# Kernel optimization log

Measured on AMD Instinct MI355X. Metric: run time of the kernel, lower is better.

The kernel has to match this reference:

```python
import jax, jax.numpy as jnp
import numpy as np

P = 16          # patch size
IMG = 384       # image size
D = 768         # model dim
DM = 3072       # mlp hidden
L = 12          # n blocks
H = 12          # n heads
DH = D // H     # head dim
NC = 1000       # n classes
B = 64          # batch
N = (IMG // P) ** 2  # 576 patches


def layernorm(x, w, b, eps=1e-5):
    m = jnp.mean(x, axis=-1, keepdims=True)
    v = jnp.mean((x - m) ** 2, axis=-1, keepdims=True)
    return (x - m) / jnp.sqrt(v + eps) * w + b


def gelu(x):
    return jax.nn.gelu(x, approximate=False)  # torch nn.GELU default (erf)


def setup_inputs() -> dict:
    key = jax.random.key(0)
    ks = iter(jax.random.split(key, 40))
    nrm = lambda shape, s=0.02: jax.random.normal(next(ks), shape, jnp.float32) * s
    return {
        "x": jax.random.normal(next(ks), (B, 3, IMG, IMG), jnp.float32),
        "class_embed": nrm((D,)),
        "pose_embed": nrm((N + 1, D)),
        "proj_w": nrm((3 * P * P, D)), "proj_b": jnp.zeros((D,), jnp.float32),
        "qkv_w": nrm((L, D, 3 * D)), "qkv_b": jnp.zeros((L, 3 * D), jnp.float32),
        "top_w": nrm((L, D, D)), "top_b": jnp.zeros((L, D), jnp.float32),
        "ln1_w": jnp.ones((L, D), jnp.float32), "ln1_b": jnp.zeros((L, D), jnp.float32),
        "ln2_w": jnp.ones((L, D), jnp.float32), "ln2_b": jnp.zeros((L, D), jnp.float32),
        "mlp_w1": nrm((L, D, DM)), "mlp_b1": jnp.zeros((L, DM), jnp.float32),
        "mlp_w2": nrm((L, DM, D)), "mlp_b2": jnp.zeros((L, D), jnp.float32),
        "ln3_w": jnp.ones((D,), jnp.float32), "ln3_b": jnp.zeros((D,), jnp.float32),
        "head_w1": nrm((D, DM)), "head_b1": jnp.zeros((DM,), jnp.float32),
        "head_w2": nrm((DM, NC)), "head_b2": jnp.zeros((NC,), jnp.float32),
    }


def reference(x, class_embed, pose_embed, proj_w, proj_b, qkv_w, qkv_b,
              top_w, top_b, ln1_w, ln1_b, ln2_w, ln2_b,
              mlp_w1, mlp_b1, mlp_w2, mlp_b2, ln3_w, ln3_b,
              head_w1, head_b1, head_w2, head_b2):
    Bx = x.shape[0]
    # _slice_patch: torch unfold(dim2).unfold(dim3) -> (B,C,N,P,P) -> permute -> flatten (C,Ph,Pw order)
    patches = x.reshape(Bx, 3, IMG // P, P, IMG // P, P)
    patches = patches.transpose(0, 2, 4, 1, 3, 5).reshape(Bx, N, 3 * P * P)
    patch_embed = patches @ proj_w + proj_b  # (B, N, D)
    cls = jnp.broadcast_to(class_embed, (Bx, 1, D))
    z = jnp.concatenate([cls, patch_embed], axis=1) + pose_embed  # (B, N+1, D)

    scale = DH ** 0.5
    for i in range(L):
        # MSA branch (note: source computes attention over the HEAD axis per token, HxH)
        h = layernorm(z, ln1_w[i], ln1_b[i])
        qkv = h @ qkv_w[i] + qkv_b[i]
        q, k, v = jnp.split(qkv, 3, axis=-1)
        q = q.reshape(Bx, N + 1, H, DH)
        k = k.reshape(Bx, N + 1, H, DH)
        v = v.reshape(Bx, N + 1, H, DH)
        A = jax.nn.softmax(jnp.einsum('bnhd,bngd->bnhg', q, k) / scale, axis=-1)
        o = jnp.einsum('bnhg,bngd->bnhd', A, v).reshape(Bx, N + 1, D)
        z = o @ top_w[i] + top_b[i] + z
        # MLP branch (GELU after both linears, per source MLP)
        h2 = layernorm(z, ln2_w[i], ln2_b[i])
        m = gelu(gelu(h2 @ mlp_w1[i] + mlp_b1[i]) @ mlp_w2[i] + mlp_b2[i])
        z = m + z

    y = layernorm(z[:, 0], ln3_w, ln3_b)  # (B, D)
    logit = gelu(gelu(y @ head_w1 + head_b1) @ head_w2 + head_b2)  # pretraining cls_head = MLP
    return logit
```

## Files before the change

### kernel.cpp

```cpp
#include <hip/hip_runtime.h>

typedef unsigned short u16;
typedef unsigned int u32;
typedef __bf16 bf16x8 __attribute__((ext_vector_type(8)));
typedef float f32x4 __attribute__((ext_vector_type(4)));

#define D_    768
#define DM_   3072
#define NL_   12
#define NT_   577
#define NP_   576
#define B_    64
#define MREAL (B_*NT_)
#define MPAD2 37120
#define NC_   1000
#define IMG_  384

__device__ __forceinline__ float bf2f(u16 v){
  union { unsigned u; float f; } c; c.u = ((unsigned)v) << 16; return c.f;
}
__device__ __forceinline__ u16 f2bf(float f){
  union { float f; unsigned u; } c; c.f = f;
  unsigned r = c.u + 0x7FFFu + ((c.u >> 16) & 1u);
  return (u16)(r >> 16);
}
__device__ __forceinline__ float gelu_f(float x){
  return 0.5f * x * (1.0f + erff(x * 0.70710678118654752f));
}
__device__ __forceinline__ void gload16(const void* g, void* l){
  __builtin_amdgcn_global_load_lds((const __attribute__((address_space(1))) void*)g,
                                   (__attribute__((address_space(3))) void*)l, 16, 0, 0);
}

#define SB_ __builtin_amdgcn_sched_barrier(0)

template<int EPI>
__global__ __launch_bounds__(512, 1) void gemm256_k(
    const u16* __restrict__ A, const u16* __restrict__ Bt,
    const float* __restrict__ bias, const float* __restrict__ res,
    void* __restrict__ outv, int K, int ldo, int nbn)
{
  __shared__ u16 lds[2][2][256*64];
  const int tid = threadIdx.x;
  const int l   = tid & 63;
  const int wid = tid >> 6;
  const int wm  = wid >> 2, wn = wid & 3;
  const int lrow = l & 15;

  const int nwg = gridDim.x;
  const int q = nwg >> 3, r = nwg & 7;
  const int xcd = blockIdx.x & 7, o = blockIdx.x >> 3;
  const int wg = (xcd < r ? xcd * (q + 1) : r * (q + 1) + (xcd - r) * q) + o;
  const int bm = wg / nbn, bn = wg % nbn;

  const int cs8 = ((tid & 7) ^ ((tid >> 3) & 7)) * 8;
  const int rb  = tid >> 3;
  const u16* aP[4]; const u16* bP[4];
  #pragma unroll
  for (int i = 0; i < 4; i++) {
    aP[i] = A  + (size_t)(bm*256 + rb + 64*i) * K + cs8;
    bP[i] = Bt + (size_t)(bn*256 + rb + 64*i) * K + cs8;
  }
  const int ldst = tid * 8;

  f32x4 acc[8][4];
  #pragma unroll
  for (int i = 0; i < 8; i++)
    #pragma unroll
    for (int j = 0; j < 4; j++) acc[i][j] = {0.f, 0.f, 0.f, 0.f};

  const int nk = K >> 6;
  #pragma unroll
  for (int i = 0; i < 4; i++) {
    gload16(aP[i], &lds[0][0][ldst + i*4096]);
    gload16(bP[i], &lds[0][1][ldst + i*4096]);
    aP[i] += 64; bP[i] += 64;
  }

  const int sw  = (lrow & 7) << 4;
  const int g16 = (l >> 4) << 4;

  for (int t = 0; t < nk; ++t) {
    const int cur = t & 1;
    const bool pre = (t + 1 < nk);
    u16* dA = &lds[cur^1][0][0];
    u16* dB = &lds[cur^1][1][0];

    if (pre) {
      gload16(aP[0], dA + ldst);
      gload16(aP[1], dA + ldst + 4096);
    }
    SB_;
    if (pre) asm volatile("s_waitcnt vmcnt(2)" ::: "memory");
    else     asm volatile("s_waitcnt vmcnt(0)" ::: "memory");
    SB_;
    __builtin_amdgcn_s_barrier();
    SB_;

    const char* As_ = (const char*)&lds[cur][0][0];
    const char* Bs_ = (const char*)&lds[cur][1][0];
    bf16x8 af[4], bfr[4];

    {
      const int kb = g16;
      #pragma unroll
      for (int ni = 0; ni < 4; ni++)
        bfr[ni] = *(const bf16x8*)(Bs_ + ((wn*64 + ni*16 + lrow) << 7) + (kb ^ sw));
      #pragma unroll
      for (int mi = 0; mi < 4; mi++)
        af[mi] = *(const bf16x8*)(As_ + ((wm*128 + mi*16 + lrow) << 7) + (kb ^ sw));
      if (pre) {
        gload16(aP[2], dA + ldst + 8192);
        gload16(aP[3], dA + ldst + 12288);
      }
      asm volatile("s_waitcnt lgkmcnt(0)" ::: "memory");
      SB_;
      __builtin_amdgcn_s_setprio(1);
      #pragma unroll
      for (int mi = 0; mi < 4; mi++)
        #pragma unroll
        for (int ni = 0; ni < 4; ni++)
          acc[mi][ni] = __builtin_amdgcn_mfma_f32_16x16x32_bf16(af[mi], bfr[ni], acc[mi][ni], 0, 0, 0);
      __builtin_amdgcn_s_setprio(0);
      SB_;
      __builtin_amdgcn_s_barrier();
      SB_;
    }
    {
      const int kb = g16;
      #pragma unroll
      for (int mi = 0; mi < 4; mi++)
        af[mi] = *(const bf16x8*)(As_ + ((wm*128 + (mi+4)*16 + lrow) << 7) + (kb ^ sw));
      if (pre) {
        gload16(bP[0], dB + ldst);
        gload16(bP[1], dB + ldst + 4096);
      }
      asm volatile("s_waitcnt lgkmcnt(0)" ::: "memory");
      SB_;
      __builtin_amdgcn_s_setprio(1);
      #pragma unroll
      for (int mi = 0; mi < 4; mi++)
        #pragma unroll
        for (int ni = 0; ni < 4; ni++)
          acc[mi+4][ni] = __builtin_amdgcn_mfma_f32_16x16x32_bf16(af[mi], bfr[ni], acc[mi+4][ni], 0, 0, 0);
      __builtin_amdgcn_s_setprio(0);
      SB_;
      __builtin_amdgcn_s_barrier();
      SB_;
    }
    {
      const int kb = 64 | g16;
      #pragma unroll
      for (int ni = 0; ni < 4; ni++)
        bfr[ni] = *(const bf16x8*)(Bs_ + ((wn*64 + ni*16 + lrow) << 7) + (kb ^ sw));
      #pragma unroll
      for (int mi = 0; mi < 4; mi++)
        af[mi] = *(const bf16x8*)(As_ + ((wm*128 + mi*16 + lrow) << 7) + (kb ^ sw));
      if (pre) {
        gload16(bP[2], dB + ldst + 8192);
        gload16(bP[3], dB + ldst + 12288);
      }
      asm volatile("s_waitcnt lgkmcnt(0)" ::: "memory");
      SB_;
      __builtin_amdgcn_s_setprio(1);
      #pragma unroll
      for (int mi = 0; mi < 4; mi++)
        #pragma unroll
        for (int ni = 0; ni < 4; ni++)
          acc[mi][ni] = __builtin_amdgcn_mfma_f32_16x16x32_bf16(af[mi], bfr[ni], acc[mi][ni], 0, 0, 0);
      __builtin_amdgcn_s_setprio(0);
      SB_;
      __builtin_amdgcn_s_barrier();
      SB_;
    }
    {
      const int kb = 64 | g16;
      #pragma unroll
      for (int mi = 0; mi < 4; mi++)
        af[mi] = *(const bf16x8*)(As_ + ((wm*128 + (mi+4)*16 + lrow) << 7) + (kb ^ sw));
      asm volatile("s_waitcnt lgkmcnt(0)" ::: "memory");
      SB_;
      __builtin_amdgcn_s_setprio(1);
      #pragma unroll
      for (int mi = 0; mi < 4; mi++)
        #pragma unroll
        for (int ni = 0; ni < 4; ni++)
          acc[mi+4][ni] = __builtin_amdgcn_mfma_f32_16x16x32_bf16(af[mi], bfr[ni], acc[mi+4][ni], 0, 0, 0);
      __builtin_amdgcn_s_setprio(0);
      SB_;
      __builtin_amdgcn_s_barrier();
      SB_;
    }
    if (pre) {
      #pragma unroll
      for (int i = 0; i < 4; i++) { aP[i] += 64; bP[i] += 64; }
    }
  }

  const int orow0 = bm*256 + wm*128;
  const int ocol0 = bn*256 + wn*64;
  #pragma unroll
  for (int mi = 0; mi < 8; mi++) {
    #pragma unroll
    for (int ni = 0; ni < 4; ni++) {
      const int col = ocol0 + ni*16 + (l & 15);
      const float bv = bias[col];
      #pragma unroll
      for (int r2 = 0; r2 < 4; r2++) {
        const int row = orow0 + mi*16 + (l >> 4)*4 + r2;
        const float v = acc[mi][ni][r2] + bv;
        const size_t idx = (size_t)row * ldo + col;
        if constexpr (EPI == 0) ((u16*)outv)[idx] = f2bf(v);
        else if constexpr (EPI == 1) ((float*)outv)[idx] = v + res[idx];
        else if constexpr (EPI == 2) ((u16*)outv)[idx] = f2bf(gelu_f(v));
        else if constexpr (EPI == 3) ((float*)outv)[idx] = gelu_f(v) + res[idx];
        else if constexpr (EPI == 4) ((float*)outv)[idx] = v;
      }
    }
  }
}

template<int EPI>
__global__ __launch_bounds__(256) void gemm_k(
    const u16* __restrict__ A, const u16* __restrict__ Bt,
    const float* __restrict__ bias, const float* __restrict__ res,
    void* __restrict__ outv, int K, int ldo, int nbn, int Ms, int Ns)
{
  __shared__ u16 As[128*64];
  __shared__ u16 Bs[128*64];
  const int tid = threadIdx.x;
  const int l   = tid & 63;
  const int w   = tid >> 6;
  const int wm  = w >> 1, wn = w & 1;
  const int lrow = l & 15;

  const int nwg = gridDim.x;
  const int q = nwg >> 3, r = nwg & 7;
  const int xcd = blockIdx.x & 7, o = blockIdx.x >> 3;
  const int wg = (xcd < r ? xcd * (q + 1) : r * (q + 1) + (xcd - r) * q) + o;
  const int bm = wg / nbn, bn = wg % nbn;

  const int cs8 = ((tid & 7) ^ ((tid >> 3) & 7)) * 8;
  const int rb  = tid >> 3;
  const size_t abase = (size_t)bm * 128 * K;
  const size_t bbase = (size_t)bn * 128 * K;
  size_t aoff[4], boff[4];
  #pragma unroll
  for (int i = 0; i < 4; i++) {
    aoff[i] = abase + (size_t)(rb + 32 * i) * K + cs8;
    boff[i] = bbase + (size_t)(rb + 32 * i) * K + cs8;
  }

  const int colA = (l >> 4) << 4;
  const int sw   = (lrow & 7) << 4;

  f32x4 acc[4][4];
  #pragma unroll
  for (int i = 0; i < 4; i++)
    #pragma unroll
    for (int j = 0; j < 4; j++) acc[i][j] = {0.f, 0.f, 0.f, 0.f};

  const int nk = K >> 6;
  for (int kt = 0; kt < nk; ++kt) {
    const int koff = kt * 64;
    #pragma unroll
    for (int i = 0; i < 4; i++) {
      gload16(A  + aoff[i] + koff, As + tid * 8 + i * 2048);
      gload16(Bt + boff[i] + koff, Bs + tid * 8 + i * 2048);
    }
    __syncthreads();
    #pragma unroll
    for (int kk = 0; kk < 2; kk++) {
      bf16x8 af[4], bfr[4];
      #pragma unroll
      for (int mi = 0; mi < 4; mi++)
        af[mi] = *(const bf16x8*)((const char*)As +
                  ((wm*64 + mi*16 + lrow) << 7) + (((kk << 6) | colA) ^ sw));
      #pragma unroll
      for (int ni = 0; ni < 4; ni++)
        bfr[ni] = *(const bf16x8*)((const char*)Bs +
                  ((wn*64 + ni*16 + lrow) << 7) + (((kk << 6) | colA) ^ sw));
      #pragma unroll
      for (int mi = 0; mi < 4; mi++)
        #pragma unroll
        for (int ni = 0; ni < 4; ni++)
          acc[mi][ni] = __builtin_amdgcn_mfma_f32_16x16x32_bf16(af[mi], bfr[ni], acc[mi][ni], 0, 0, 0);
    }
    __syncthreads();
  }

  const int orow0 = bm*128 + wm*64;
  const int ocol0 = bn*128 + wn*64;
  #pragma unroll
  for (int mi = 0; mi < 4; mi++) {
    #pragma unroll
    for (int ni = 0; ni < 4; ni++) {
      #pragma unroll
      for (int r2 = 0; r2 < 4; r2++) {
        const int row = orow0 + mi*16 + (l >> 4)*4 + r2;
        const int col = ocol0 + ni*16 + (l & 15);
        float bv;
        if constexpr (EPI == 5) bv = (col < Ns) ? bias[col] : 0.f;
        else bv = bias[col];
        const float v = acc[mi][ni][r2] + bv;
        const size_t idx = (size_t)row * ldo + col;
        if constexpr (EPI == 2) ((u16*)outv)[idx] = f2bf(gelu_f(v));
        else if constexpr (EPI == 5) {
          if (row < Ms && col < Ns) ((float*)outv)[(size_t)row * Ns + col] = gelu_f(v);
        }
      }
    }
  }
}

__global__ void wconv_k(const float* __restrict__ W, u16* __restrict__ Wt,
                        int K, int N)
{
  __shared__ float tile[32][33];
  const int n0 = blockIdx.x * 32, k0 = blockIdx.y * 32;
  const int tx = threadIdx.x, ty = threadIdx.y;
  #pragma unroll
  for (int r = 0; r < 4; r++) {
    const int kk = k0 + ty + r*8;
    const int nn = n0 + tx;
    tile[ty + r*8][tx] = (nn < N) ? W[(size_t)kk * N + nn] : 0.f;
  }
  __syncthreads();
  #pragma unroll
  for (int r = 0; r < 4; r++) {
    const int nn = n0 + ty + r*8;
    Wt[(size_t)nn * K + k0 + tx] = f2bf(tile[tx][ty + r*8]);
  }
}

__global__ void patchify_k(const float* __restrict__ x, u16* __restrict__ hb)
{
  const int blk = blockIdx.x;
  const int b = blk / NP_, p = blk % NP_;
  const int pr = p / 24, pc = p % 24;
  const size_t row = (size_t)b * NT_ + 1 + p;
  #pragma unroll
  for (int u = 0; u < 3; u++) {
    const int j  = threadIdx.x + u * 256;
    const int c  = j >> 8, ph = (j >> 4) & 15, pw = j & 15;
    const float v = x[((size_t)(b*3 + c) * IMG_ + pr*16 + ph) * IMG_ + pc*16 + pw];
    hb[row * D_ + j] = f2bf(v);
  }
}

__global__ void posecls_k(float* __restrict__ z, const float* __restrict__ ce,
                          const float* __restrict__ pe)
{
  const int row = blockIdx.x;
  const int t = row % NT_;
  const size_t base = (size_t)row * D_;
  #pragma unroll
  for (int u = 0; u < 3; u++) {
    const int j = threadIdx.x + u * 256;
    if (t == 0) z[base + j] = ce[j] + pe[j];
    else        z[base + j] += pe[(size_t)t * D_ + j];
  }
}

__global__ void ln_k(const float* __restrict__ z, const float* __restrict__ w,
                     const float* __restrict__ b, u16* __restrict__ out)
{
  const int row = blockIdx.x * 4 + (threadIdx.x >> 6);
  const int l = threadIdx.x & 63;
  const float4* zr = (const float4*)(z + (size_t)row * D_);
  float4 xq[3];
  float s = 0.f;
  #pragma unroll
  for (int j = 0; j < 3; j++) {
    xq[j] = zr[j*64 + l];
    s += xq[j].x + xq[j].y + xq[j].z + xq[j].w;
  }
  #pragma unroll
  for (int m = 1; m < 64; m <<= 1) s += __shfl_xor(s, m, 64);
  const float mean = s * (1.0f / 768.0f);
  float ss = 0.f;
  #pragma unroll
  for (int j = 0; j < 3; j++) {
    const float dx = xq[j].x-mean, dy = xq[j].y-mean, dz = xq[j].z-mean, dw = xq[j].w-mean;
    ss += dx*dx + dy*dy + dz*dz + dw*dw;
  }
  #pragma unroll
  for (int m = 1; m < 64; m <<= 1) ss += __shfl_xor(ss, m, 64);
  const float rinv = rsqrtf(ss * (1.0f / 768.0f) + 1e-5f);
  const size_t ob = (size_t)row * D_;
  #pragma unroll
  for (int j = 0; j < 3; j++) {
    const int c = (j*64 + l) * 4;
    const float4 wv = *(const float4*)(w + c);
    const float4 bv = *(const float4*)(b + c);
    ushort4 ov;
    ov.x = f2bf((xq[j].x - mean) * rinv * wv.x + bv.x);
    ov.y = f2bf((xq[j].y - mean) * rinv * wv.y + bv.y);
    ov.z = f2bf((xq[j].z - mean) * rinv * wv.z + bv.z);
    ov.w = f2bf((xq[j].w - mean) * rinv * wv.w + bv.w);
    *(ushort4*)(out + ob + c) = ov;
  }
}

__global__ void lncls_k(const float* __restrict__ z, const float* __restrict__ w,
                        const float* __restrict__ b, u16* __restrict__ out)
{
  const int row = blockIdx.x * 4 + (threadIdx.x >> 6);
  const int l = threadIdx.x & 63;
  const size_t ob = (size_t)row * D_;
  if (row >= B_) {
    #pragma unroll
    for (int j = 0; j < 12; j++) out[ob + j*64 + l] = 0;
    return;
  }
  const float* zr = z + (size_t)row * NT_ * D_;
  float xv[12];
  float s = 0.f;
  #pragma unroll
  for (int j = 0; j < 12; j++) { xv[j] = zr[j*64 + l]; s += xv[j]; }
  #pragma unroll
  for (int m = 1; m < 64; m <<= 1) s += __shfl_xor(s, m, 64);
  const float mean = s * (1.0f / 768.0f);
  float ss = 0.f;
  #pragma unroll
  for (int j = 0; j < 12; j++) { const float d = xv[j] - mean; ss += d * d; }
  #pragma unroll
  for (int m = 1; m < 64; m <<= 1) ss += __shfl_xor(ss, m, 64);
  const float rinv = rsqrtf(ss * (1.0f / 768.0f) + 1e-5f);
  #pragma unroll
  for (int j = 0; j < 12; j++) {
    const int cidx = j*64 + l;
    out[ob + cidx] = f2bf((xv[j] - mean) * rinv * w[cidx] + b[cidx]);
  }
}

__global__ __launch_bounds__(256) void attn_k(const u16* __restrict__ qkv,
                                              u16* __restrict__ o)
{
  const int tok = (blockIdx.x * 256 + threadIdx.x) >> 6;
  const int l  = threadIdx.x & 63;
  const int g  = l >> 4, li = l & 15;
  const size_t rb = (size_t)tok * (3 * D_);

  f32x4 s = {0.f, 0.f, 0.f, 0.f};
  #pragma unroll
  for (int kt = 0; kt < 2; kt++) {
    const bf16x8 ka = *(const bf16x8*)(qkv + rb + D_ + li*64 + g*8 + kt*32);
    const bf16x8 qb = *(const bf16x8*)(qkv + rb +      li*64 + g*8 + kt*32);
    s = __builtin_amdgcn_mfma_f32_16x16x32_bf16(ka, qb, s, 0, 0, 0);
  }

  float sv[4];
  #pragma unroll
  for (int r2 = 0; r2 < 4; r2++) sv[r2] = s[r2] * 0.125f;
  float mx = (g < 3) ? fmaxf(fmaxf(sv[0], sv[1]), fmaxf(sv[2], sv[3])) : -1e30f;
  mx = fmaxf(mx, __shfl_xor(mx, 16, 64));
  mx = fmaxf(mx, __shfl_xor(mx, 32, 64));
  float p[4], den = 0.f;
  #pragma unroll
  for (int r2 = 0; r2 < 4; r2++) {
    p[r2] = (g < 3) ? __expf(sv[r2] - mx) : 0.f;
    den += p[r2];
  }
  den += __shfl_xor(den, 16, 64);
  den += __shfl_xor(den, 32, 64);
  const float rden = 1.0f / den;
  #pragma unroll
  for (int r2 = 0; r2 < 4; r2++) p[r2] *= rden;

  const u32 pk01 = ((u32)f2bf(p[1]) << 16) | f2bf(p[0]);
  const u32 pk23 = ((u32)f2bf(p[3]) << 16) | f2bf(p[2]);

  const int srcA = (li + (g << 5)) & 63;
  const int srcB = (srcA + 16) & 63;
  u32 b0 = (u32)__shfl((int)pk01, srcA, 64);
  u32 b1 = (u32)__shfl((int)pk23, srcA, 64);
  u32 b2 = (u32)__shfl((int)pk01, srcB, 64);
  u32 b3 = (u32)__shfl((int)pk23, srcB, 64);
  if (g >= 2) { b0 = 0; b1 = 0; b2 = 0; b3 = 0; }
  union { u32 u[4]; bf16x8 v; } pb;
  pb.u[0] = b0; pb.u[1] = b1; pb.u[2] = b2; pb.u[3] = b3;

  const size_t ob = (size_t)tok * D_;
  #pragma unroll
  for (int t = 0; t < 4; t++) {
    union { u16 a[8]; bf16x8 v; } va;
    #pragma unroll
    for (int jp = 0; jp < 8; jp++) {
      const int j = g * 8 + jp;
      va.a[jp] = (j < 12) ? qkv[rb + 2*D_ + j*64 + t*16 + li] : (u16)0;
    }
    f32x4 oac = {0.f, 0.f, 0.f, 0.f};
    oac = __builtin_amdgcn_mfma_f32_16x16x32_bf16(va.v, pb.v, oac, 0, 0, 0);
    if (li < 12) {
      ushort4 ov;
      ov.x = f2bf(oac[0]); ov.y = f2bf(oac[1]);
      ov.z = f2bf(oac[2]); ov.w = f2bf(oac[3]);
      *(ushort4*)(o + ob + li*64 + t*16 + g*4) = ov;
    }
  }
}

extern "C" void kernel_launch(void* const* d_in, const int* in_sizes, int n_in,
                              void* d_out, int out_size, void* d_ws, size_t ws_size,
                              hipStream_t stream)
{
  const float* x    = (const float*)d_in[0];
  const float* ce   = (const float*)d_in[1];
  const float* pe   = (const float*)d_in[2];
  const float* pw   = (const float*)d_in[3];
  const float* pb   = (const float*)d_in[4];
  const float* qkvw = (const float*)d_in[5];
  const float* qkvb = (const float*)d_in[6];
  const float* topw = (const float*)d_in[7];
  const float* topb = (const float*)d_in[8];
  const float* l1w  = (const float*)d_in[9];
  const float* l1b  = (const float*)d_in[10];
  const float* l2w  = (const float*)d_in[11];
  const float* l2b  = (const float*)d_in[12];
  const float* w1   = (const float*)d_in[13];
  const float* b1   = (const float*)d_in[14];
  const float* w2   = (const float*)d_in[15];
  const float* b2   = (const float*)d_in[16];
  const float* l3w  = (const float*)d_in[17];
  const float* l3b  = (const float*)d_in[18];
  const float* hw1  = (const float*)d_in[19];
  const float* hb1  = (const float*)d_in[20];
  const float* hw2  = (const float*)d_in[21];
  const float* hb2  = (const float*)d_in[22];

  char* ws = (char*)d_ws;
  constexpr size_t SZ_Z  = (size_t)MPAD2 * D_ * 4;
  constexpr size_t SZ_HB = (size_t)MPAD2 * D_ * 2;
  constexpr size_t SZ_QM = (size_t)MPAD2 * DM_ * 2;
  constexpr size_t SZ_WB = (size_t)DM_ * 1024 * 2;
  constexpr size_t SZ_YB = (size_t)128 * D_ * 2;
  float* z  = (float*)ws;
  u16*   hb = (u16*)(ws + SZ_Z);
  u16*   qm = (u16*)(ws + SZ_Z + SZ_HB);
  u16*   wb = (u16*)(ws + SZ_Z + SZ_HB + SZ_QM);
  u16*   yb = (u16*)(ws + SZ_Z + SZ_HB + SZ_QM + SZ_WB);
  u16*   t1 = (u16*)(ws + SZ_Z + SZ_HB + SZ_QM + SZ_WB + SZ_YB);

  const dim3 blk(256);
  const dim3 blk5(512);
  const dim3 wblk(32, 8);
  const int MT2 = MPAD2 / 256;

  patchify_k<<<B_ * NP_, blk, 0, stream>>>(x, hb);
  wconv_k<<<dim3(D_/32, D_/32), wblk, 0, stream>>>(pw, wb, D_, D_);
  gemm256_k<4><<<3*MT2, blk5, 0, stream>>>(hb, wb, pb, nullptr, z, D_, D_, 3);
  posecls_k<<<MREAL, blk, 0, stream>>>(z, ce, pe);

  for (int i = 0; i < NL_; i++) {
    ln_k<<<MPAD2/4, blk, 0, stream>>>(z, l1w + i*D_, l1b + i*D_, hb);
    wconv_k<<<dim3(3*D_/32, D_/32), wblk, 0, stream>>>(qkvw + (size_t)i*D_*3*D_, wb, D_, 3*D_);
    gemm256_k<0><<<9*MT2, blk5, 0, stream>>>(hb, wb, qkvb + i*3*D_, nullptr, qm, D_, 3*D_, 9);
    attn_k<<<MREAL/4, blk, 0, stream>>>(qm, hb);
    wconv_k<<<dim3(D_/32, D_/32), wblk, 0, stream>>>(topw + (size_t)i*D_*D_, wb, D_, D_);
    gemm256_k<1><<<3*MT2, blk5, 0, stream>>>(hb, wb, topb + i*D_, z, z, D_, D_, 3);
    ln_k<<<MPAD2/4, blk, 0, stream>>>(z, l2w + i*D_, l2b + i*D_, hb);
    wconv_k<<<dim3(DM_/32, D_/32), wblk, 0, stream>>>(w1 + (size_t)i*D_*DM_, wb, D_, DM_);
    gemm256_k<2><<<12*MT2, blk5, 0, stream>>>(hb, wb, b1 + i*DM_, nullptr, qm, D_, DM_, 12);
    wconv_k<<<dim3(D_/32, DM_/32), wblk, 0, stream>>>(w2 + (size_t)i*DM_*D_, wb, DM_, D_);
    gemm256_k<3><<<3*MT2, blk5, 0, stream>>>(qm, wb, b2 + i*D_, z, z, DM_, D_, 3);
  }

  lncls_k<<<32, blk, 0, stream>>>(z, l3w, l3b, yb);
  wconv_k<<<dim3(DM_/32, D_/32), wblk, 0, stream>>>(hw1, wb, D_, DM_);
  gemm_k<2><<<24, blk, 0, stream>>>(yb, wb, hb1, nullptr, t1, D_, DM_, 24, 0, 0);
  wconv_k<<<dim3(1024/32, DM_/32), wblk, 0, stream>>>(hw2, wb, DM_, NC_);
  gemm_k<5><<<8, blk, 0, stream>>>(t1, wb, hb2, nullptr, (float*)d_out, DM_, 1024, 8, B_, NC_);
}
```

Before: 11.24 ms.

## Emit LayerNorm output in MFMA-fragment packed layout and load A directly to registers

LayerNorm now writes its bf16 output in a pre-packed layout matching the MFMA 16x32 A-fragment order, so the QKV and MLP-up GEMMs can load A straight from global memory into registers. This removes the A tile from LDS and halves LDS use and LDS traffic in those GEMMs. A fragments are double-buffered in registers across the k loop. The cost is more register pressure and uncoalesced-per-wave global loads for A with no LDS reuse across waves, and LayerNorm rereads z a second time.

Result: slower. 12.02 ms (+7.0%).

```diff
diff --git a/kernel.cpp b/kernel.cpp
--- a/kernel.cpp
+++ b/kernel.cpp
@@ -31,8 +31,132 @@
   __builtin_amdgcn_global_load_lds((const __attribute__((address_space(1))) void*)g,
                                    (__attribute__((address_space(3))) void*)l, 16, 0, 0);
 }
-
 #define SB_ __builtin_amdgcn_sched_barrier(0)
+
+template<int EPI>
+__global__ __launch_bounds__(512, 1) void gemmPA_k(
+    const u16* __restrict__ Apk, const u16* __restrict__ Bt,
+    const float* __restrict__ bias,
+    void* __restrict__ outv, int K, int ldo, int nbn)
+{
+  __shared__ u16 Bs[2][16384];
+  const int tid = threadIdx.x;
+  const int l   = tid & 63;
+  const int wid = tid >> 6;
+  const int wm  = wid >> 2, wn = wid & 3;
+  const int lrow = l & 15;
+
+  const int nwg = gridDim.x;
+  const int q = nwg >> 3, r = nwg & 7;
+  const int xcd = blockIdx.x & 7, o = blockIdx.x >> 3;
+  const int wg = (xcd < r ? xcd * (q + 1) : r * (q + 1) + (xcd - r) * q) + o;
+  const int bm = wg / nbn, bn = wg % nbn;
+
+  const int cs8 = ((tid & 7) ^ ((tid >> 3) & 7)) * 8;
+  const int rb  = tid >> 3;
+  const u16* bP[4];
+  #pragma unroll
+  for (int i = 0; i < 4; i++)
+    bP[i] = Bt + (size_t)(bn*256 + rb + 64*i) * K + cs8;
+  const int ldst = tid * 8;
+
+  const int KT = K >> 5;
+  const u16* aBase = Apk + (size_t)(bm*16 + wm*8) * KT * 512 + (size_t)l * 8;
+
+  const int sw  = (lrow & 7) << 4;
+  const int g16 = (l >> 4) << 4;
+
+  f32x4 acc[8][4];
+  #pragma unroll
+  for (int i = 0; i < 8; i++)
+    #pragma unroll
+    for (int j = 0; j < 4; j++) acc[i][j] = {0.f, 0.f, 0.f, 0.f};
+
+  const int nk = K >> 6;
+
+  #pragma unroll
+  for (int i = 0; i < 4; i++) { gload16(bP[i], &Bs[0][ldst + i*4096]); bP[i] += 64; }
+  bf16x8 Ae[8], Ao[8];
+  #pragma unroll
+  for (int mi = 0; mi < 8; mi++) Ae[mi] = *(const bf16x8*)(aBase + ((size_t)mi*KT + 0)*512);
+  #pragma unroll
+  for (int mi = 0; mi < 8; mi++) Ao[mi] = *(const bf16x8*)(aBase + ((size_t)mi*KT + 1)*512);
+
+  for (int t = 0; t < nk; ++t) {
+    const int cur = t & 1;
+    const bool pre = (t + 1 < nk);
+    if (pre) {
+      #pragma unroll
+      for (int i = 0; i < 4; i++) { gload16(bP[i], &Bs[cur^1][ldst + i*4096]); bP[i] += 64; }
+    }
+    SB_;
+    if (pre) asm volatile("s_waitcnt vmcnt(20)" ::: "memory");
+    else     asm volatile("s_waitcnt vmcnt(16)" ::: "memory");
+    SB_;
+    __builtin_amdgcn_s_barrier();
+    SB_;
+    const char* Bb = (const char*)&Bs[cur][0];
+    bf16x8 bfr[4];
+    #pragma unroll
+    for (int ni = 0; ni < 4; ni++)
+      bfr[ni] = *(const bf16x8*)(Bb + ((wn*64 + ni*16 + lrow) << 7) + (g16 ^ sw));
+    asm volatile("s_waitcnt lgkmcnt(0)" ::: "memory");
+    SB_;
+    __builtin_amdgcn_s_setprio(1);
+    #pragma unroll
+    for (int mi = 0; mi < 8; mi++)
+      #pragma unroll
+      for (int ni = 0; ni < 4; ni++)
+        acc[mi][ni] = __builtin_amdgcn_mfma_f32_16x16x32_bf16(Ae[mi], bfr[ni], acc[mi][ni], 0, 0, 0);
+    __builtin_amdgcn_s_setprio(0);
+    SB_;
+    if (pre) {
+      #pragma unroll
+      for (int mi = 0; mi < 8; mi++)
+        Ae[mi] = *(const bf16x8*)(aBase + ((size_t)mi*KT + 2*(t+1))*512);
+    }
+    #pragma unroll
+    for (int ni = 0; ni < 4; ni++)
+      bfr[ni] = *(const bf16x8*)(Bb + ((wn*64 + ni*16 + lrow) << 7) + ((64 | g16) ^ sw));
+    asm volatile("s_waitcnt lgkmcnt(0)" ::: "memory");
+    SB_;
+    __builtin_amdgcn_s_setprio(1);
+    #pragma unroll
+    for (int mi = 0; mi < 8; mi++)
+      #pragma unroll
+      for (int ni = 0; ni < 4; ni++)
+        acc[mi][ni] = __builtin_amdgcn_mfma_f32_16x16x32_bf16(Ao[mi], bfr[ni], acc[mi][ni], 0, 0, 0);
+    __builtin_amdgcn_s_setprio(0);
+    SB_;
+    if (pre) {
+      #pragma unroll
+      for (int mi = 0; mi < 8; mi++)
+        Ao[mi] = *(const bf16x8*)(aBase + ((size_t)mi*KT + 2*(t+1) + 1)*512);
+    }
+    SB_;
+    __builtin_amdgcn_s_barrier();
+    SB_;
+  }
+
+  const int orow0 = bm*256 + wm*128;
+  const int ocol0 = bn*256 + wn*64;
+  #pragma unroll
+  for (int mi = 0; mi < 8; mi++) {
+    #pragma unroll
+    for (int ni = 0; ni < 4; ni++) {
+      const int col = ocol0 + ni*16 + (l & 15);
+      const float bv = bias[col];
+      #pragma unroll
+      for (int r2 = 0; r2 < 4; r2++) {
+        const int row = orow0 + mi*16 + (l >> 4)*4 + r2;
+        const float v = acc[mi][ni][r2] + bv;
+        const size_t idx = (size_t)row * ldo + col;
+        if constexpr (EPI == 0) ((u16*)outv)[idx] = f2bf(v);
+        else if constexpr (EPI == 2) ((u16*)outv)[idx] = f2bf(gelu_f(v));
+      }
+    }
+  }
+}
 
 template<int EPI>
 __global__ __launch_bounds__(512, 1) void gemm256_k(
@@ -210,9 +334,7 @@
         const int row = orow0 + mi*16 + (l >> 4)*4 + r2;
         const float v = acc[mi][ni][r2] + bv;
         const size_t idx = (size_t)row * ldo + col;
-        if constexpr (EPI == 0) ((u16*)outv)[idx] = f2bf(v);
-        else if constexpr (EPI == 1) ((float*)outv)[idx] = v + res[idx];
-        else if constexpr (EPI == 2) ((u16*)outv)[idx] = f2bf(gelu_f(v));
+        if constexpr (EPI == 1) ((float*)outv)[idx] = v + res[idx];
         else if constexpr (EPI == 3) ((float*)outv)[idx] = gelu_f(v) + res[idx];
         else if constexpr (EPI == 4) ((float*)outv)[idx] = v;
       }
@@ -362,43 +484,66 @@
   }
 }
 
-__global__ void ln_k(const float* __restrict__ z, const float* __restrict__ w,
-                     const float* __restrict__ b, u16* __restrict__ out)
-{
-  const int row = blockIdx.x * 4 + (threadIdx.x >> 6);
-  const int l = threadIdx.x & 63;
-  const float4* zr = (const float4*)(z + (size_t)row * D_);
-  float4 xq[3];
-  float s = 0.f;
-  #pragma unroll
-  for (int j = 0; j < 3; j++) {
-    xq[j] = zr[j*64 + l];
-    s += xq[j].x + xq[j].y + xq[j].z + xq[j].w;
-  }
-  #pragma unroll
-  for (int m = 1; m < 64; m <<= 1) s += __shfl_xor(s, m, 64);
-  const float mean = s * (1.0f / 768.0f);
-  float ss = 0.f;
-  #pragma unroll
-  for (int j = 0; j < 3; j++) {
-    const float dx = xq[j].x-mean, dy = xq[j].y-mean, dz = xq[j].z-mean, dw = xq[j].w-mean;
-    ss += dx*dx + dy*dy + dz*dz + dw*dw;
-  }
-  #pragma unroll
-  for (int m = 1; m < 64; m <<= 1) ss += __shfl_xor(ss, m, 64);
-  const float rinv = rsqrtf(ss * (1.0f / 768.0f) + 1e-5f);
-  const size_t ob = (size_t)row * D_;
-  #pragma unroll
-  for (int j = 0; j < 3; j++) {
-    const int c = (j*64 + l) * 4;
-    const float4 wv = *(const float4*)(w + c);
-    const float4 bv = *(const float4*)(b + c);
-    ushort4 ov;
-    ov.x = f2bf((xq[j].x - mean) * rinv * wv.x + bv.x);
-    ov.y = f2bf((xq[j].y - mean) * rinv * wv.y + bv.y);
-    ov.z = f2bf((xq[j].z - mean) * rinv * wv.z + bv.z);
-    ov.w = f2bf((xq[j].w - mean) * rinv * wv.w + bv.w);
-    *(ushort4*)(out + ob + c) = ov;
+__global__ void ln_pk(const float* __restrict__ z, const float* __restrict__ w,
+                      const float* __restrict__ b, u16* __restrict__ out)
+{
+  __shared__ float st[16][2];
+  const int blk = blockIdx.x;
+  const int tid = threadIdx.x;
+  const int l = tid & 63, w4 = tid >> 6;
+
+  for (int rr = 0; rr < 4; rr++) {
+    const int lr = w4*4 + rr;
+    const float4* zr = (const float4*)(z + ((size_t)blk*16 + lr) * D_);
+    float4 xq[3];
+    float s = 0.f;
+    #pragma unroll
+    for (int j = 0; j < 3; j++) {
+      xq[j] = zr[j*64 + l];
+      s += xq[j].x + xq[j].y + xq[j].z + xq[j].w;
+    }
+    #pragma unroll
+    for (int m = 1; m < 64; m <<= 1) s += __shfl_xor(s, m, 64);
+    const float mean = s * (1.0f / 768.0f);
+    float ss = 0.f;
+    #pragma unroll
+    for (int j = 0; j < 3; j++) {
+      const float dx = xq[j].x-mean, dy = xq[j].y-mean, dz = xq[j].z-mean, dw = xq[j].w-mean;
+      ss += dx*dx + dy*dy + dz*dz + dw*dw;
+    }
+    #pragma unroll
+    for (int m = 1; m < 64; m <<= 1) ss += __shfl_xor(ss, m, 64);
+    if (l == 0) {
+      st[lr][0] = mean;
+      st[lr][1] = rsqrtf(ss * (1.0f / 768.0f) + 1e-5f);
+    }
+  }
+  __syncthreads();
+
+  #pragma unroll
+  for (int i = 0; i < 6; i++) {
+    const int c = tid + i*256;
+    const int kt = c >> 6, lane = c & 63;
+    const int lr = lane & 15, g = (lane >> 4);
+    const int k0 = kt*32 + g*8;
+    const float* zp = z + ((size_t)blk*16 + lr) * D_ + k0;
+    const float4 a0 = *(const float4*)zp;
+    const float4 a1 = *(const float4*)(zp + 4);
+    const float4 w0 = *(const float4*)(w + k0);
+    const float4 w1 = *(const float4*)(w + k0 + 4);
+    const float4 b0 = *(const float4*)(b + k0);
+    const float4 b1 = *(const float4*)(b + k0 + 4);
+    const float mean = st[lr][0], rinv = st[lr][1];
+    u16 ov[8];
+    ov[0] = f2bf((a0.x - mean) * rinv * w0.x + b0.x);
+    ov[1] = f2bf((a0.y - mean) * rinv * w0.y + b0.y);
+    ov[2] = f2bf((a0.z - mean) * rinv * w0.z + b0.z);
+    ov[3] = f2bf((a0.w - mean) * rinv * w0.w + b0.w);
+    ov[4] = f2bf((a1.x - mean) * rinv * w1.x + b1.x);
+    ov[5] = f2bf((a1.y - mean) * rinv * w1.y + b1.y);
+    ov[6] = f2bf((a1.z - mean) * rinv * w1.z + b1.z);
+    ov[7] = f2bf((a1.w - mean) * rinv * w1.w + b1.w);
+    *(uint4*)(out + ((size_t)(blk*24 + kt)*64 + lane)*8) = *(const uint4*)ov;
   }
 }
 
@@ -553,15 +698,15 @@
   posecls_k<<<MREAL, blk, 0, stream>>>(z, ce, pe);
 
   for (int i = 0; i < NL_; i++) {
-    ln_k<<<MPAD2/4, blk, 0, stream>>>(z, l1w + i*D_, l1b + i*D_, hb);
+    ln_pk<<<MPAD2/16, blk, 0, stream>>>(z, l1w + i*D_, l1b + i*D_, hb);
     wconv_k<<<dim3(3*D_/32, D_/32), wblk, 0, stream>>>(qkvw + (size_t)i*D_*3*D_, wb, D_, 3*D_);
-    gemm256_k<0><<<9*MT2, blk5, 0, stream>>>(hb, wb, qkvb + i*3*D_, nullptr, qm, D_, 3*D_, 9);
+    gemmPA_k<0><<<9*MT2, blk5, 0, stream>>>(hb, wb, qkvb + i*3*D_, qm, D_, 3*D_, 9);
     attn_k<<<MREAL/4, blk, 0, stream>>>(qm, hb);
     wconv_k<<<dim3(D_/32, D_/32), wblk, 0, stream>>>(topw + (size_t)i*D_*D_, wb, D_, D_);
     gemm256_k<1><<<3*MT2, blk5, 0, stream>>>(hb, wb, topb + i*D_, z, z, D_, D_, 3);
-    ln_k<<<MPAD2/4, blk, 0, stream>>>(z, l2w + i*D_, l2b + i*D_, hb);
+    ln_pk<<<MPAD2/16, blk, 0, stream>>>(z, l2w + i*D_, l2b + i*D_, hb);
     wconv_k<<<dim3(DM_/32, D_/32), wblk, 0, stream>>>(w1 + (size_t)i*D_*DM_, wb, D_, DM_);
-    gemm256_k<2><<<12*MT2, blk5, 0, stream>>>(hb, wb, b1 + i*DM_, nullptr, qm, D_, DM_, 12);
+    gemmPA_k<2><<<12*MT2, blk5, 0, stream>>>(hb, wb, b1 + i*DM_, qm, D_, DM_, 12);
     wconv_k<<<dim3(D_/32, DM_/32), wblk, 0, stream>>>(w2 + (size_t)i*DM_*D_, wb, DM_, D_);
     gemm256_k<3><<<3*MT2, blk5, 0, stream>>>(qm, wb, b2 + i*D_, z, z, DM_, D_, 3);
   }
```

## Add 128x128 triple-buffered GEMM for QKV and MLP-up projections

Applied to the files above, without the earlier changes.

Adds a new 256-thread GEMM kernel with 128x128 tiles, a 3-slot LDS ring fed by direct global-to-LDS loads, swizzled LDS layout, and multiple workgroups per CU. QKV and first MLP GEMMs (bf16 output epilogues) switch from the 256x256 single-occupancy kernel to this one. The intent is to hide memory latency through deeper prefetch and higher occupancy. The trade-off is less operand reuse per tile, so more global and LDS traffic.

Result: no change. 11.33 ms (+0.8%).

```diff
diff --git a/kernel.cpp b/kernel.cpp
--- a/kernel.cpp
+++ b/kernel.cpp
@@ -31,8 +31,126 @@
   __builtin_amdgcn_global_load_lds((const __attribute__((address_space(1))) void*)g,
                                    (__attribute__((address_space(3))) void*)l, 16, 0, 0);
 }
-
 #define SB_ __builtin_amdgcn_sched_barrier(0)
+
+template<int EPI>
+__global__ __launch_bounds__(256, 3) void gemmR_k(
+    const u16* __restrict__ A, const u16* __restrict__ Bt,
+    const float* __restrict__ bias,
+    void* __restrict__ outv, int K, int ldo, int nbn)
+{
+  __shared__ u16 ring[3][2][4096];
+  const int tid = threadIdx.x;
+  const int l   = tid & 63;
+  const int w   = tid >> 6;
+  const int wm  = w >> 1, wn = w & 1;
+  const int lrow = l & 15;
+  const int g2   = l >> 4;
+
+  const int nwg = gridDim.x;
+  const int q = nwg >> 3, r = nwg & 7;
+  const int xcd = blockIdx.x & 7, o = blockIdx.x >> 3;
+  const int wg = (xcd < r ? xcd * (q + 1) : r * (q + 1) + (xcd - r) * q) + o;
+  const int bm = wg / nbn, bn = wg % nbn;
+
+  const int rp0  = tid >> 3;
+  const int rodd = (tid >> 2) & 1;
+  const int scol = ((tid & 3) ^ (rp0 & 3)) * 8;
+  const u16* aS[2]; const u16* bS[2];
+  #pragma unroll
+  for (int i = 0; i < 2; i++) {
+    const int row = (rp0 + 32*i) * 2 + rodd;
+    aS[i] = A  + (size_t)(bm*128 + row) * K + scol;
+    bS[i] = Bt + (size_t)(bn*128 + row) * K + scol;
+  }
+  const int dst = tid * 8;
+
+  int afo[4], bfo[4];
+  #pragma unroll
+  for (int mi = 0; mi < 4; mi++) {
+    const int ar = wm*64 + mi*16 + lrow;
+    afo[mi] = (ar >> 1)*128 + (ar & 1)*64 + ((g2 ^ ((ar >> 1) & 3)) << 4);
+    const int br = wn*64 + mi*16 + lrow;
+    bfo[mi] = (br >> 1)*128 + (br & 1)*64 + ((g2 ^ ((br >> 1) & 3)) << 4);
+  }
+
+  f32x4 acc[4][4];
+  #pragma unroll
+  for (int i = 0; i < 4; i++)
+    #pragma unroll
+    for (int j = 0; j < 4; j++) acc[i][j] = {0.f, 0.f, 0.f, 0.f};
+
+  const int nt = K >> 5;
+
+#define STG_R(t_) { \
+    const int sl_ = (t_) % 3; const int ko_ = (t_) * 32; \
+    gload16(aS[0] + ko_, &ring[sl_][0][dst]); \
+    gload16(aS[1] + ko_, &ring[sl_][0][dst + 2048]); \
+    gload16(bS[0] + ko_, &ring[sl_][1][dst]); \
+    gload16(bS[1] + ko_, &ring[sl_][1][dst + 2048]); }
+
+#define CMP_R(t_) { \
+    const int sl_ = (t_) % 3; \
+    const char* As_ = (const char*)&ring[sl_][0][0]; \
+    const char* Bs_ = (const char*)&ring[sl_][1][0]; \
+    bf16x8 af[4], bfr[4]; \
+    _Pragma("unroll") \
+    for (int mi = 0; mi < 4; mi++) af[mi]  = *(const bf16x8*)(As_ + afo[mi]); \
+    _Pragma("unroll") \
+    for (int ni = 0; ni < 4; ni++) bfr[ni] = *(const bf16x8*)(Bs_ + bfo[ni]); \
+    asm volatile("s_waitcnt lgkmcnt(0)" ::: "memory"); \
+    SB_; \
+    __builtin_amdgcn_s_setprio(1); \
+    _Pragma("unroll") \
+    for (int mi = 0; mi < 4; mi++) \
+      _Pragma("unroll") \
+      for (int ni = 0; ni < 4; ni++) \
+        acc[mi][ni] = __builtin_amdgcn_mfma_f32_16x16x32_bf16(af[mi], bfr[ni], acc[mi][ni], 0, 0, 0); \
+    __builtin_amdgcn_s_setprio(0); \
+    SB_; \
+    __builtin_amdgcn_s_barrier(); \
+    SB_; }
+
+  STG_R(0); STG_R(1);
+
+  for (int t = 0; t < nt - 2; ++t) {
+    STG_R(t + 2);
+    SB_;
+    asm volatile("s_waitcnt vmcnt(8)" ::: "memory");
+    SB_;
+    __builtin_amdgcn_s_barrier();
+    SB_;
+    CMP_R(t);
+  }
+  SB_; asm volatile("s_waitcnt vmcnt(4)" ::: "memory"); SB_;
+  __builtin_amdgcn_s_barrier(); SB_;
+  CMP_R(nt - 2);
+  SB_; asm volatile("s_waitcnt vmcnt(0)" ::: "memory"); SB_;
+  __builtin_amdgcn_s_barrier(); SB_;
+  CMP_R(nt - 1);
+
+#undef STG_R
+#undef CMP_R
+
+  const int orow0 = bm*128 + wm*64;
+  const int ocol0 = bn*128 + wn*64;
+  #pragma unroll
+  for (int mi = 0; mi < 4; mi++) {
+    #pragma unroll
+    for (int ni = 0; ni < 4; ni++) {
+      const int col = ocol0 + ni*16 + lrow;
+      const float bv = bias[col];
+      #pragma unroll
+      for (int r2 = 0; r2 < 4; r2++) {
+        const int row = orow0 + mi*16 + g2*4 + r2;
+        const float v = acc[mi][ni][r2] + bv;
+        const size_t idx = (size_t)row * ldo + col;
+        if constexpr (EPI == 0) ((u16*)outv)[idx] = f2bf(v);
+        else if constexpr (EPI == 2) ((u16*)outv)[idx] = f2bf(gelu_f(v));
+      }
+    }
+  }
+}
 
 template<int EPI>
 __global__ __launch_bounds__(512, 1) void gemm256_k(
@@ -210,9 +328,7 @@
         const int row = orow0 + mi*16 + (l >> 4)*4 + r2;
         const float v = acc[mi][ni][r2] + bv;
         const size_t idx = (size_t)row * ldo + col;
-        if constexpr (EPI == 0) ((u16*)outv)[idx] = f2bf(v);
-        else if constexpr (EPI == 1) ((float*)outv)[idx] = v + res[idx];
-        else if constexpr (EPI == 2) ((u16*)outv)[idx] = f2bf(gelu_f(v));
+        if constexpr (EPI == 1) ((float*)outv)[idx] = v + res[idx];
         else if constexpr (EPI == 3) ((float*)outv)[idx] = gelu_f(v) + res[idx];
         else if constexpr (EPI == 4) ((float*)outv)[idx] = v;
       }
@@ -545,6 +661,7 @@
   const dim3 blk(256);
   const dim3 blk5(512);
   const dim3 wblk(32, 8);
+  const int MT1 = MPAD2 / 128;
   const int MT2 = MPAD2 / 256;
 
   patchify_k<<<B_ * NP_, blk, 0, stream>>>(x, hb);
@@ -555,13 +672,13 @@
   for (int i = 0; i < NL_; i++) {
     ln_k<<<MPAD2/4, blk, 0, stream>>>(z, l1w + i*D_, l1b + i*D_, hb);
     wconv_k<<<dim3(3*D_/32, D_/32), wblk, 0, stream>>>(qkvw + (size_t)i*D_*3*D_, wb, D_, 3*D_);
-    gemm256_k<0><<<9*MT2, blk5, 0, stream>>>(hb, wb, qkvb + i*3*D_, nullptr, qm, D_, 3*D_, 9);
+    gemmR_k<0><<<18*MT1, blk, 0, stream>>>(hb, wb, qkvb + i*3*D_, qm, D_, 3*D_, 18);
     attn_k<<<MREAL/4, blk, 0, stream>>>(qm, hb);
     wconv_k<<<dim3(D_/32, D_/32), wblk, 0, stream>>>(topw + (size_t)i*D_*D_, wb, D_, D_);
     gemm256_k<1><<<3*MT2, blk5, 0, stream>>>(hb, wb, topb + i*D_, z, z, D_, D_, 3);
     ln_k<<<MPAD2/4, blk, 0, stream>>>(z, l2w + i*D_, l2b + i*D_, hb);
     wconv_k<<<dim3(DM_/32, D_/32), wblk, 0, stream>>>(w1 + (size_t)i*D_*DM_, wb, D_, DM_);
-    gemm256_k<2><<<12*MT2, blk5, 0, stream>>>(hb, wb, b1 + i*DM_, nullptr, qm, D_, DM_, 12);
+    gemmR_k<2><<<24*MT1, blk, 0, stream>>>(hb, wb, b1 + i*DM_, qm, D_, DM_, 24);
     wconv_k<<<dim3(D_/32, DM_/32), wblk, 0, stream>>>(w2 + (size_t)i*DM_*D_, wb, DM_, D_);
     gemm256_k<3><<<3*MT2, blk5, 0, stream>>>(qm, wb, b2 + i*D_, z, z, DM_, D_, 3);
   }
```
